# Optimization experiments

Hardware: AMD Instinct MI355X
Metric: run time of the kernel (lower is better)

The kernel has to match this reference:

```python
import jax, jax.numpy as jnp
import numpy as np

T = 2048          # num tokens (prefill)
H = 4096          # hidden_size
NH = 32           # num query heads
NKV = 8           # num kv heads (GQA)
HD = H // NH      # head_dim = 128
BASE = 1000000.0  # rope_theta
NEG = -1e30


def _rope(x, positions):
    # NeoX-style rotary embedding (vLLM default). x: [T, nh, HD]
    half = HD // 2
    inv_freq = 1.0 / (BASE ** (jnp.arange(half, dtype=jnp.float32) / half))
    freqs = positions.astype(jnp.float32)[:, None] * inv_freq  # [T, half]
    cos = jnp.concatenate([jnp.cos(freqs), jnp.cos(freqs)], -1)[:, None, :]
    sin = jnp.concatenate([jnp.sin(freqs), jnp.sin(freqs)], -1)[:, None, :]
    rot = jnp.concatenate([-x[..., half:], x[..., :half]], -1)
    return x * cos + rot * sin


def setup_inputs() -> dict:
    key = jax.random.key(0)
    k1, k2, k3 = jax.random.split(key, 3)
    hidden_states = jax.random.normal(k1, (T, H), jnp.float32)
    wqkv = jax.random.normal(k2, (H, (NH + 2 * NKV) * HD), jnp.float32) * 0.02
    wo = jax.random.normal(k3, (NH * HD, H), jnp.float32) * 0.02
    positions = jnp.arange(T, dtype=jnp.int32)
    return {"positions": positions, "hidden_states": hidden_states,
            "wqkv": wqkv, "wo": wo}


def reference(positions, hidden_states, wqkv, wo):
    # fused QKV projection
    qkv = hidden_states @ wqkv                      # [T, (NH+2*NKV)*HD]
    q, k, v = jnp.split(qkv, [NH * HD, NH * HD + NKV * HD], axis=-1)
    q = q.reshape(T, NH, HD)
    k = k.reshape(T, NKV, HD)
    v = v.reshape(T, NKV, HD)
    # inline RoPE on q, k
    q = _rope(q, positions)
    k = _rope(k, positions)
    # GQA: expand kv heads to query heads
    rep = NH // NKV
    k = jnp.repeat(k, rep, axis=1)                  # [T, NH, HD]
    v = jnp.repeat(v, rep, axis=1)
    # causal scaled dot-product attention (prefill path of PagedAttention)
    scores = jnp.einsum('qhd,khd->hqk', q, k) * (HD ** -0.5)  # [NH, T, T]
    causal = positions[:, None] >= positions[None, :]          # [T, T]
    scores = jnp.where(causal[None, :, :], scores, NEG)
    probs = jax.nn.softmax(scores, axis=-1)
    attn = jnp.einsum('hqk,khd->qhd', probs, v).reshape(T, NH * HD)
    return attn @ wo
```

## Files before the change

kernel.cpp:

```cpp
#include <hip/hip_runtime.h>
#include <hip/hip_bf16.h>

typedef __attribute__((ext_vector_type(8))) short bf16x8;
typedef __attribute__((ext_vector_type(4))) float f32x4;
typedef unsigned short u16;

#define T_TOK 2048
#define HID 4096
#define NH 32
#define NKV 8
#define HD 128
#define QKVN 6144
#define KOFF 4096
#define VOFF 5120

static __device__ __forceinline__ float bf2f(u16 x) {
    union { float f; unsigned u; } v; v.u = ((unsigned)x) << 16; return v.f;
}
static __device__ __forceinline__ u16 f2bf(float f) {
    union { float f; unsigned u; } v; v.f = f;
    unsigned u = v.u;
    unsigned r = (u + 0x7fff + ((u >> 16) & 1)) >> 16;
    return (u16)r;
}

static __device__ __forceinline__ void gload16(const u16* g, u16* l) {
    __builtin_amdgcn_global_load_lds((const __attribute__((address_space(1))) void*)g,
                                     (__attribute__((address_space(3))) void*)l, 16, 0, 0);
}

__global__ __launch_bounds__(256) void convk(const float* __restrict__ in, u16* __restrict__ out) {
    int i = blockIdx.x * 256 + threadIdx.x;
    float4 v = ((const float4*)in)[i];
    ushort4 o;
    o.x = f2bf(v.x); o.y = f2bf(v.y); o.z = f2bf(v.z); o.w = f2bf(v.w);
    ((ushort4*)out)[i] = o;
}

__global__ __launch_bounds__(256) void transpk(const float* __restrict__ in, u16* __restrict__ out,
                                               int R, int C) {
    __shared__ float tile[64][65];
    int c0 = blockIdx.x * 64, r0 = blockIdx.y * 64;
    int tid = threadIdx.x;
#pragma unroll
    for (int it = 0; it < 4; ++it) {
        int ci = it * 256 + tid;
        int r = ci >> 4, c4 = (ci & 15) * 4;
        float4 v = *(const float4*)&in[(size_t)(r0 + r) * C + c0 + c4];
        tile[r][c4 + 0] = v.x; tile[r][c4 + 1] = v.y; tile[r][c4 + 2] = v.z; tile[r][c4 + 3] = v.w;
    }
    __syncthreads();
#pragma unroll
    for (int it = 0; it < 4; ++it) {
        int ci = it * 256 + tid;
        int c = ci >> 4, rq = (ci & 15) * 4;
        ushort4 o;
        o.x = f2bf(tile[rq + 0][c]); o.y = f2bf(tile[rq + 1][c]);
        o.z = f2bf(tile[rq + 2][c]); o.w = f2bf(tile[rq + 3][c]);
        *(ushort4*)&out[(size_t)(c0 + c) * R + r0 + rq] = o;
    }
}

template <int OUTF32>
__global__ __launch_bounds__(256) void gemm_bt(const u16* __restrict__ A, const u16* __restrict__ Bt,
                                               void* __restrict__ Cout, int M, int N, int K) {
    __shared__ __attribute__((aligned(16))) u16 at[128 * 64];
    __shared__ __attribute__((aligned(16))) u16 bt[128 * 64];
    int m0 = blockIdx.y * 128, n0 = blockIdx.x * 128;
    int tid = threadIdx.x;
    int lane = tid & 63, wid = tid >> 6;
    int wr = wid >> 1, wc = wid & 1;
    int l15 = lane & 15, g = lane >> 4;
    int sw = lane & 7;

    int srow = wid * 32 + (lane >> 3);
    int scol = ((lane & 7) ^ (lane >> 3)) * 8;
    const u16* agp = &A[(size_t)(m0 + srow) * K + scol];
    const u16* bgp = &Bt[(size_t)(n0 + srow) * K + scol];

    f32x4 acc[4][4];
#pragma unroll
    for (int mi = 0; mi < 4; ++mi)
#pragma unroll
        for (int ni = 0; ni < 4; ++ni) acc[mi][ni] = (f32x4){0.f, 0.f, 0.f, 0.f};

    for (int kb = 0; kb < K; kb += 64) {
        __syncthreads();
#pragma unroll
        for (int c = 0; c < 4; ++c) {
            gload16(agp + (size_t)(c * 8) * K + kb, &at[(wid * 32 + c * 8) * 64]);
            gload16(bgp + (size_t)(c * 8) * K + kb, &bt[(wid * 32 + c * 8) * 64]);
        }
        __syncthreads();
#pragma unroll
        for (int ks = 0; ks < 2; ++ks) {
            bf16x8 af[4], bfr[4];
#pragma unroll
            for (int mi = 0; mi < 4; ++mi)
                af[mi] = *(const bf16x8*)&at[(wr * 64 + mi * 16 + l15) * 64 + (((ks * 4 + g) ^ sw) * 8)];
#pragma unroll
            for (int ni = 0; ni < 4; ++ni)
                bfr[ni] = *(const bf16x8*)&bt[(wc * 64 + ni * 16 + l15) * 64 + (((ks * 4 + g) ^ sw) * 8)];
#pragma unroll
            for (int mi = 0; mi < 4; ++mi)
#pragma unroll
                for (int ni = 0; ni < 4; ++ni)
                    acc[mi][ni] = __builtin_amdgcn_mfma_f32_16x16x32_bf16(af[mi], bfr[ni], acc[mi][ni], 0, 0, 0);
        }
    }
#pragma unroll
    for (int mi = 0; mi < 4; ++mi)
#pragma unroll
        for (int ni = 0; ni < 4; ++ni)
#pragma unroll
            for (int i = 0; i < 4; ++i) {
                int row = m0 + wr * 64 + mi * 16 + g * 4 + i;
                int col = n0 + wc * 64 + ni * 16 + l15;
                float v = acc[mi][ni][i];
                if (OUTF32) ((float*)Cout)[(size_t)row * N + col] = v;
                else        ((u16*)Cout)[(size_t)row * N + col] = f2bf(v);
            }
}

__global__ __launch_bounds__(256) void ropek(u16* __restrict__ qkvb, const int* __restrict__ positions) {
    int t = blockIdx.x;
    float pos = (float)positions[t];
#pragma unroll
    for (int it = 0; it < 10; ++it) {
        int ci = it * 256 + threadIdx.x;
        int hh = ci >> 6, d = ci & 63;
        int base = (hh < NH) ? hh * HD : KOFF + (hh - NH) * HD;
        size_t off = (size_t)t * QKVN + base + d;
        float x1 = bf2f(qkvb[off]);
        float x2 = bf2f(qkvb[off + 64]);
        float inv = powf(1.0e6f, -(float)d * (1.0f / 64.0f));
        float fr = pos * inv;
        float s = sinf(fr), c = cosf(fr);
        qkvb[off]      = f2bf(x1 * c - x2 * s);
        qkvb[off + 64] = f2bf(x2 * c + x1 * s);
    }
}

__global__ __launch_bounds__(256) void vtranspk(const u16* __restrict__ qkvb, u16* __restrict__ vT) {
    __shared__ __attribute__((aligned(16))) u16 tile[64][136];
    int kvh = blockIdx.x, t0 = blockIdx.y * 64;
    int tid = threadIdx.x;
#pragma unroll
    for (int it = 0; it < 4; ++it) {
        int ci = it * 256 + tid;
        int r = ci >> 4, c8 = (ci & 15) * 8;
        *(bf16x8*)&tile[r][c8] = *(const bf16x8*)&qkvb[(size_t)(t0 + r) * QKVN + VOFF + kvh * HD + c8];
    }
    __syncthreads();
#pragma unroll
    for (int it = 0; it < 4; ++it) {
        int ci = it * 256 + tid;
        int d = ci >> 3, tc = (ci & 7) * 8;
        union { bf16x8 v; u16 u[8]; } o;
#pragma unroll
        for (int e = 0; e < 8; ++e) o.u[e] = tile[tc + e][d];
        *(bf16x8*)&vT[((size_t)kvh * HD + d) * T_TOK + t0 + tc] = o.v;
    }
}

__global__ __launch_bounds__(256) void attnk(const u16* __restrict__ qkvb, const u16* __restrict__ vT,
                                             u16* __restrict__ attnb) {
    __shared__ __attribute__((aligned(16))) u16 kt_[64 * 136];
    __shared__ __attribute__((aligned(16))) u16 vt_[128 * 72];
    __shared__ __attribute__((aligned(16))) u16 pl_[4 * 16 * 72];
    int h = blockIdx.x, qt = 31 - blockIdx.y;
    int kvh = h >> 2;
    int q0 = qt * 64;
    int tid = threadIdx.x, lane = tid & 63, wid = tid >> 6;
    int l15 = lane & 15, g = lane >> 4;
    const float scale = 0.08838834764831845f;

    int kr = tid >> 4, kc = (tid & 15) * 8;
    int vd = tid >> 3, vc = (tid & 7) * 8;
    const u16* kbase = qkvb + KOFF + (size_t)kvh * HD + kc;
    const u16* vbase = vT + ((size_t)kvh * HD) * T_TOK + vc;

    bf16x8 qf[4];
    int qrow = q0 + wid * 16 + l15;
#pragma unroll
    for (int ks = 0; ks < 4; ++ks)
        qf[ks] = *(const bf16x8*)&qkvb[(size_t)qrow * QKVN + h * HD + ks * 32 + g * 8];

    f32x4 o[8];
#pragma unroll
    for (int df = 0; df < 8; ++df) o[df] = (f32x4){0.f, 0.f, 0.f, 0.f};
    float m_run[4], l_run[4];
#pragma unroll
    for (int i = 0; i < 4; ++i) { m_run[i] = -3.0e38f; l_run[i] = 0.f; }

    bf16x8 kreg[4], vreg[4];
#pragma unroll
    for (int it = 0; it < 4; ++it)
        kreg[it] = *(const bf16x8*)&kbase[(size_t)(it * 16 + kr) * QKVN];
#pragma unroll
    for (int it = 0; it < 4; ++it)
        vreg[it] = *(const bf16x8*)&vbase[(size_t)(it * 32 + vd) * T_TOK];
#pragma unroll
    for (int it = 0; it < 4; ++it) *(bf16x8*)&kt_[(it * 16 + kr) * 136 + kc] = kreg[it];
#pragma unroll
    for (int it = 0; it < 4; ++it) *(bf16x8*)&vt_[(it * 32 + vd) * 72 + vc] = vreg[it];
    {
        int ktl = (1 <= qt) ? 1 : qt;
#pragma unroll
        for (int it = 0; it < 4; ++it)
            kreg[it] = *(const bf16x8*)&kbase[(size_t)(ktl * 64 + it * 16 + kr) * QKVN];
#pragma unroll
        for (int it = 0; it < 4; ++it)
            vreg[it] = *(const bf16x8*)&vbase[(size_t)(it * 32 + vd) * T_TOK + ktl * 64];
    }
    __syncthreads();

    for (int kt2 = 0; kt2 <= qt; ++kt2) {
        int kvb = kt2 * 64;

        f32x4 s[4];
#pragma unroll
        for (int nf = 0; nf < 4; ++nf) s[nf] = (f32x4){0.f, 0.f, 0.f, 0.f};
        __builtin_amdgcn_s_setprio(1);
#pragma unroll
        for (int ks = 0; ks < 4; ++ks) {
#pragma unroll
            for (int nf = 0; nf < 4; ++nf) {
                bf16x8 bfr = *(const bf16x8*)&kt_[(nf * 16 + l15) * 136 + ks * 32 + g * 8];
                s[nf] = __builtin_amdgcn_mfma_f32_16x16x32_bf16(qf[ks], bfr, s[nf], 0, 0, 0);
            }
        }
        __builtin_amdgcn_s_setprio(0);

        float mrow[4];
#pragma unroll
        for (int i = 0; i < 4; ++i) {
            int qr = q0 + wid * 16 + g * 4 + i;
            float mx = -3.0e38f;
#pragma unroll
            for (int nf = 0; nf < 4; ++nf) {
                int kvc = kvb + nf * 16 + l15;
                float v = s[nf][i] * scale;
                v = (kvc <= qr) ? v : -1.0e30f;
                s[nf][i] = v;
                mx = fmaxf(mx, v);
            }
            mrow[i] = mx;
        }
#pragma unroll
        for (int dd = 1; dd < 16; dd <<= 1)
#pragma unroll
            for (int i = 0; i < 4; ++i) mrow[i] = fmaxf(mrow[i], __shfl_xor(mrow[i], dd));

        int ok = 1;
#pragma unroll
        for (int i = 0; i < 4; ++i) ok &= (mrow[i] <= m_run[i] + 8.0f) ? 1 : 0;
        if (!__all(ok)) {
            float alpha[4];
#pragma unroll
            for (int i = 0; i < 4; ++i) {
                float mnew = fmaxf(m_run[i], mrow[i]);
                alpha[i] = __expf(m_run[i] - mnew);
                m_run[i] = mnew;
                l_run[i] *= alpha[i];
            }
#pragma unroll
            for (int df = 0; df < 8; ++df)
#pragma unroll
                for (int i = 0; i < 4; ++i) o[df][i] *= alpha[i];
        }

        float rsum[4] = {0.f, 0.f, 0.f, 0.f};
#pragma unroll
        for (int nf = 0; nf < 4; ++nf)
#pragma unroll
            for (int i = 0; i < 4; ++i) {
                float p = __expf(s[nf][i] - m_run[i]);
                rsum[i] += p;
                pl_[wid * 1152 + (g * 4 + i) * 72 + nf * 16 + l15] = f2bf(p);
            }
#pragma unroll
        for (int dd = 1; dd < 16; dd <<= 1)
#pragma unroll
            for (int i = 0; i < 4; ++i) rsum[i] += __shfl_xor(rsum[i], dd);
#pragma unroll
        for (int i = 0; i < 4; ++i) l_run[i] += rsum[i];

        __builtin_amdgcn_s_setprio(1);
#pragma unroll
        for (int ks2 = 0; ks2 < 2; ++ks2) {
            bf16x8 af = *(const bf16x8*)&pl_[wid * 1152 + l15 * 72 + ks2 * 32 + g * 8];
#pragma unroll
            for (int df = 0; df < 8; ++df) {
                bf16x8 bfr = *(const bf16x8*)&vt_[(df * 16 + l15) * 72 + ks2 * 32 + g * 8];
                o[df] = __builtin_amdgcn_mfma_f32_16x16x32_bf16(af, bfr, o[df], 0, 0, 0);
            }
        }
        __builtin_amdgcn_s_setprio(0);

        if (kt2 < qt) {
            __syncthreads();
#pragma unroll
            for (int it = 0; it < 4; ++it) *(bf16x8*)&kt_[(it * 16 + kr) * 136 + kc] = kreg[it];
#pragma unroll
            for (int it = 0; it < 4; ++it) *(bf16x8*)&vt_[(it * 32 + vd) * 72 + vc] = vreg[it];
            int ktl = (kt2 + 2 <= qt) ? kt2 + 2 : qt;
#pragma unroll
            for (int it = 0; it < 4; ++it)
                kreg[it] = *(const bf16x8*)&kbase[(size_t)(ktl * 64 + it * 16 + kr) * QKVN];
#pragma unroll
            for (int it = 0; it < 4; ++it)
                vreg[it] = *(const bf16x8*)&vbase[(size_t)(it * 32 + vd) * T_TOK + ktl * 64];
            __syncthreads();
        }
    }

#pragma unroll
    for (int df = 0; df < 8; ++df)
#pragma unroll
        for (int i = 0; i < 4; ++i) {
            int qr = q0 + wid * 16 + g * 4 + i;
            int col = h * HD + df * 16 + l15;
            attnb[(size_t)qr * (NH * HD) + col] = f2bf(o[df][i] / l_run[i]);
        }
}

extern "C" void kernel_launch(void* const* d_in, const int* in_sizes, int n_in,
                              void* d_out, int out_size, void* d_ws, size_t ws_size,
                              hipStream_t stream) {
    const int*   positions = (const int*)d_in[0];
    const float* hs        = (const float*)d_in[1];
    const float* wqkv      = (const float*)d_in[2];
    const float* wo        = (const float*)d_in[3];
    float* out = (float*)d_out;

    char* ws = (char*)d_ws;
    u16* hsb   = (u16*)(ws);
    u16* wqkvT = (u16*)(ws + 16777216);
    u16* woT   = (u16*)(ws + 16777216 + 50331648);
    u16* qkvb  = (u16*)(ws + 16777216 + 50331648 + 33554432);
    u16* vT    = (u16*)(ws + 16777216 + 50331648 + 33554432 + 25165824);
    u16* attnb = hsb;

    convk<<<8192, 256, 0, stream>>>(hs, hsb);
    transpk<<<dim3(96, 64), 256, 0, stream>>>(wqkv, wqkvT, HID, QKVN);
    transpk<<<dim3(64, 64), 256, 0, stream>>>(wo, woT, HID, HID);

    gemm_bt<0><<<dim3(48, 16), 256, 0, stream>>>(hsb, wqkvT, qkvb, T_TOK, QKVN, HID);

    ropek<<<T_TOK, 256, 0, stream>>>(qkvb, positions);

    vtranspk<<<dim3(NKV, 32), 256, 0, stream>>>(qkvb, vT);

    attnk<<<dim3(NH, 32), 256, 0, stream>>>(qkvb, vT, attnb);

    gemm_bt<1><<<dim3(32, 16), 256, 0, stream>>>(attnb, woT, out, T_TOK, HID, HID);
}
```

Baseline: 371.4 us.

## Replace GEMM with 8-wave 256-row tiles and 4-stage pipelined LDS loads

Replaces the single-buffered 128x128 GEMM with a 512-thread kernel using 256xBN tiles, BK=32 and a 4-deep LDS ring buffer. Global loads for k-step g+3 are issued while MFMAs run on step g, with explicit vmcnt waits and barriers, and s_setprio raises priority around the MFMA block. The two projections now use 192 and 256 blocks, which is fewer than the 256 CUs, and this trades grid parallelism for reuse per tile. RoPE also computes each token's cos/sin table once in shared memory instead of per element.

```diff
diff --git a/kernel.cpp b/kernel.cpp
--- a/kernel.cpp
+++ b/kernel.cpp
@@ -61,70 +61,119 @@
     }
 }
 
-template <int OUTF32>
-__global__ __launch_bounds__(256) void gemm_bt(const u16* __restrict__ A, const u16* __restrict__ Bt,
-                                               void* __restrict__ Cout, int M, int N, int K) {
-    __shared__ __attribute__((aligned(16))) u16 at[128 * 64];
-    __shared__ __attribute__((aligned(16))) u16 bt[128 * 64];
-    int m0 = blockIdx.y * 128, n0 = blockIdx.x * 128;
-    int tid = threadIdx.x;
-    int lane = tid & 63, wid = tid >> 6;
-    int wr = wid >> 1, wc = wid & 1;
-    int l15 = lane & 15, g = lane >> 4;
-    int sw = lane & 7;
-
-    int srow = wid * 32 + (lane >> 3);
-    int scol = ((lane & 7) ^ (lane >> 3)) * 8;
-    const u16* agp = &A[(size_t)(m0 + srow) * K + scol];
-    const u16* bgp = &Bt[(size_t)(n0 + srow) * K + scol];
-
-    f32x4 acc[4][4];
-#pragma unroll
-    for (int mi = 0; mi < 4; ++mi)
-#pragma unroll
-        for (int ni = 0; ni < 4; ++ni) acc[mi][ni] = (f32x4){0.f, 0.f, 0.f, 0.f};
-
-    for (int kb = 0; kb < K; kb += 64) {
-        __syncthreads();
-#pragma unroll
-        for (int c = 0; c < 4; ++c) {
-            gload16(agp + (size_t)(c * 8) * K + kb, &at[(wid * 32 + c * 8) * 64]);
-            gload16(bgp + (size_t)(c * 8) * K + kb, &bt[(wid * 32 + c * 8) * 64]);
-        }
-        __syncthreads();
-#pragma unroll
-        for (int ks = 0; ks < 2; ++ks) {
-            bf16x8 af[4], bfr[4];
-#pragma unroll
-            for (int mi = 0; mi < 4; ++mi)
-                af[mi] = *(const bf16x8*)&at[(wr * 64 + mi * 16 + l15) * 64 + (((ks * 4 + g) ^ sw) * 8)];
-#pragma unroll
-            for (int ni = 0; ni < 4; ++ni)
-                bfr[ni] = *(const bf16x8*)&bt[(wc * 64 + ni * 16 + l15) * 64 + (((ks * 4 + g) ^ sw) * 8)];
-#pragma unroll
-            for (int mi = 0; mi < 4; ++mi)
-#pragma unroll
-                for (int ni = 0; ni < 4; ++ni)
-                    acc[mi][ni] = __builtin_amdgcn_mfma_f32_16x16x32_bf16(af[mi], bfr[ni], acc[mi][ni], 0, 0, 0);
-        }
-    }
-#pragma unroll
-    for (int mi = 0; mi < 4; ++mi)
-#pragma unroll
-        for (int ni = 0; ni < 4; ++ni)
+template <int BN, int OUTF32>
+__global__ __launch_bounds__(512) void gemm8p(const u16* __restrict__ A, const u16* __restrict__ Bt,
+                                              void* __restrict__ Cout, int M, int N, int K) {
+    constexpr int BM = 256, BK = 32;
+    constexpr int WN = BN / 4;
+    constexpr int NF = WN / 16;
+    constexpr int ACALLS = 2;
+    constexpr int BCALLS = BN / 128;
+    constexpr int CALLS = ACALLS + BCALLS;
+    constexpr int PHASES = (BN == 256) ? 2 : 1;
+    constexpr int AFR = 8 / PHASES;
+    constexpr int CPP = CALLS / PHASES;
+    constexpr int ABUF = BM * BK;
+    constexpr int BBUF = BN * BK;
+    constexpr int BUFSZ = ABUF + BBUF;
+
+    __shared__ __attribute__((aligned(16))) u16 lds[4 * BUFSZ];
+
+    int bid = blockIdx.x;
+    int m0 = (bid & 7) * BM, n0 = (bid >> 3) * BN;
+    int tid = threadIdx.x, lane = tid & 63, wid = tid >> 6;
+    int wm = wid >> 2, wn = wid & 3;
+    int l15 = lane & 15, g4 = lane >> 4;
+    int srow = lane >> 2;
+    int sslot = (lane & 3) ^ (srow & 3);
+    int NK = K / BK;
+
+    auto STAGE = [&](int kt, int c) {
+        u16* base = &lds[(kt & 3) * BUFSZ];
+        size_t kcol = (size_t)kt * BK + sslot * 8;
+        if (c < ACALLS) {
+            int ch = wid * ACALLS + c;
+            gload16(&A[(size_t)(m0 + ch * 16 + srow) * K + kcol], base + ch * 512);
+        } else {
+            int ch = wid * BCALLS + (c - ACALLS);
+            gload16(&Bt[(size_t)(n0 + ch * 16 + srow) * K + kcol], base + ABUF + ch * 512);
+        }
+    };
+
+    f32x4 acc[8][NF];
+#pragma unroll
+    for (int i = 0; i < 8; ++i)
+#pragma unroll
+        for (int j = 0; j < NF; ++j) acc[i][j] = (f32x4){0.f, 0.f, 0.f, 0.f};
+
+    for (int t = 0; t < 3; ++t)
+        for (int c = 0; c < CALLS; ++c) STAGE(t, c);
+    asm volatile("s_waitcnt vmcnt(%0)" :: "i"(2 * CALLS) : "memory");
+    __builtin_amdgcn_s_barrier();
+    __builtin_amdgcn_sched_barrier(0);
+
+    for (int g = 0; g < NK; ++g) {
+        const u16* ab = &lds[(g & 3) * BUFSZ];
+        const u16* bb = ab + ABUF;
+        int swz = (g4 ^ (l15 & 3)) * 8;
+#pragma unroll
+        for (int p = 0; p < PHASES; ++p) {
+            bf16x8 af[AFR], bfr[NF];
+#pragma unroll
+            for (int i = 0; i < AFR; ++i)
+                af[i] = *(const bf16x8*)&ab[(wm * 128 + (p * AFR + i) * 16 + l15) * BK + swz];
+#pragma unroll
+            for (int j = 0; j < NF; ++j)
+                bfr[j] = *(const bf16x8*)&bb[(wn * WN + j * 16 + l15) * BK + swz];
+            if (g + 3 < NK) {
+#pragma unroll
+                for (int c = 0; c < CPP; ++c) STAGE(g + 3, p * CPP + c);
+            }
+            __builtin_amdgcn_s_barrier();
+            __builtin_amdgcn_s_setprio(1);
+#pragma unroll
+            for (int i = 0; i < AFR; ++i)
+#pragma unroll
+                for (int j = 0; j < NF; ++j)
+                    acc[p * AFR + i][j] =
+                        __builtin_amdgcn_mfma_f32_16x16x32_bf16(af[i], bfr[j], acc[p * AFR + i][j], 0, 0, 0);
+            __builtin_amdgcn_s_setprio(0);
+            if (p == PHASES - 1) {
+                if (g < NK - 3)       asm volatile("s_waitcnt vmcnt(%0)" :: "i"(2 * CALLS) : "memory");
+                else if (g == NK - 3) asm volatile("s_waitcnt vmcnt(%0)" :: "i"(CALLS) : "memory");
+                else if (g == NK - 2) asm volatile("s_waitcnt vmcnt(0)" ::: "memory");
+            }
+            __builtin_amdgcn_s_barrier();
+            __builtin_amdgcn_sched_barrier(0);
+        }
+    }
+
+#pragma unroll
+    for (int mi = 0; mi < 8; ++mi)
+#pragma unroll
+        for (int j = 0; j < NF; ++j)
 #pragma unroll
             for (int i = 0; i < 4; ++i) {
-                int row = m0 + wr * 64 + mi * 16 + g * 4 + i;
-                int col = n0 + wc * 64 + ni * 16 + l15;
-                float v = acc[mi][ni][i];
+                int row = m0 + wm * 128 + mi * 16 + g4 * 4 + i;
+                int col = n0 + wn * WN + j * 16 + l15;
+                float v = acc[mi][j][i];
                 if (OUTF32) ((float*)Cout)[(size_t)row * N + col] = v;
                 else        ((u16*)Cout)[(size_t)row * N + col] = f2bf(v);
             }
 }
 
 __global__ __launch_bounds__(256) void ropek(u16* __restrict__ qkvb, const int* __restrict__ positions) {
+    __shared__ float cs_[64], sn_[64];
     int t = blockIdx.x;
     float pos = (float)positions[t];
+    if (threadIdx.x < 64) {
+        int d = threadIdx.x;
+        float inv = exp2f(-(float)d * (19.931568569324174f / 64.0f));
+        float fr = pos * inv;
+        cs_[d] = cosf(fr);
+        sn_[d] = sinf(fr);
+    }
+    __syncthreads();
 #pragma unroll
     for (int it = 0; it < 10; ++it) {
         int ci = it * 256 + threadIdx.x;
@@ -133,9 +182,7 @@
         size_t off = (size_t)t * QKVN + base + d;
         float x1 = bf2f(qkvb[off]);
         float x2 = bf2f(qkvb[off + 64]);
-        float inv = powf(1.0e6f, -(float)d * (1.0f / 64.0f));
-        float fr = pos * inv;
-        float s = sinf(fr), c = cosf(fr);
+        float s = sn_[d], c = cs_[d];
         qkvb[off]      = f2bf(x1 * c - x2 * s);
         qkvb[off + 64] = f2bf(x2 * c + x1 * s);
     }
@@ -346,7 +393,7 @@
     transpk<<<dim3(96, 64), 256, 0, stream>>>(wqkv, wqkvT, HID, QKVN);
     transpk<<<dim3(64, 64), 256, 0, stream>>>(wo, woT, HID, HID);
 
-    gemm_bt<0><<<dim3(48, 16), 256, 0, stream>>>(hsb, wqkvT, qkvb, T_TOK, QKVN, HID);
+    gemm8p<256, 0><<<dim3(192), 512, 0, stream>>>(hsb, wqkvT, qkvb, T_TOK, QKVN, HID);
 
     ropek<<<T_TOK, 256, 0, stream>>>(qkvb, positions);
 
@@ -354,5 +401,5 @@
 
     attnk<<<dim3(NH, 32), 256, 0, stream>>>(qkvb, vT, attnb);
 
-    gemm_bt<1><<<dim3(32, 16), 256, 0, stream>>>(attnb, woT, out, T_TOK, HID, HID);
-}
+    gemm8p<128, 1><<<dim3(256), 512, 0, stream>>>(attnb, woT, out, T_TOK, HID, HID);
+}
```

Measured after the change: 389.3 us. +4.8%, slower.
